# Performance work log

Measured on AMD Instinct MI355X. Metric: run time of the kernel, lower is better.

Reference implementation:

```python
import jax, jax.numpy as jnp
import numpy as np

DIM = 384; H = 64; W = 64; WS = 4; NH = 6; SHIFT = 2
L = WS * WS          # 16 tokens per window
DH = DIM // NH       # 64
SCALE = DH ** -0.5
MLP_H = int(DIM * 4.0)
NW = (H // WS) * (W // WS)


def _ln(x, g, b):
    m = x.mean(-1, keepdims=True)
    v = ((x - m) ** 2).mean(-1, keepdims=True)
    return (x - m) / jnp.sqrt(v + 1e-5) * g + b


def _win(x, B):
    # (B, N, C) -> (B*nW, L, C)
    x = x.reshape(B, H // WS, WS, W // WS, WS, DIM)
    x = x.transpose(0, 1, 3, 2, 4, 5)
    return x.reshape(B * NW, L, DIM)


def _unwin(xw, B):
    # (B*nW, L, C) -> (B, N, C)
    x = xw.reshape(B, H // WS, W // WS, WS, WS, DIM)
    x = x.transpose(0, 1, 3, 2, 4, 5)
    return x.reshape(B, H * W, DIM)


def _build_mask():
    img = np.zeros((H, W))
    slices = [slice(0, -WS), slice(-WS, -SHIFT), slice(-SHIFT, None)]
    cnt = 0
    for hs in slices:
        for ws_ in slices:
            img[hs, ws_] = cnt
            cnt += 1
    mw = img.reshape(H // WS, WS, W // WS, WS).transpose(0, 2, 1, 3).reshape(-1, L)
    am = mw[:, None, :] - mw[:, :, None]          # (nW, L, L)
    am = np.where(am != 0, -100.0, 0.0).astype(np.float32)
    return jnp.asarray(am)

ATTN_MASK = _build_mask()  # (nW, L, L)


def setup_inputs() -> dict:
    key = jax.random.key(0)
    ks = jax.random.split(key, 16)
    n = lambda k, s: jax.random.normal(k, s, jnp.float32) * 0.02
    inp = {
        'x_main': jax.random.normal(ks[0], (16, H * W, DIM), jnp.float32),
        'x_mpmt': jax.random.normal(ks[1], (16, H * W, DIM), jnp.float32),
        'g_q': jnp.ones((DIM,)), 'b_q': jnp.zeros((DIM,)),
        'g_km': jnp.ones((DIM,)), 'b_km': jnp.zeros((DIM,)),
        'g_kp': jnp.ones((DIM,)), 'b_kp': jnp.zeros((DIM,)),
        'Wq': n(ks[2], (DIM, DIM)), 'bq': jnp.zeros((DIM,)),
        'Wk': n(ks[3], (DIM, DIM)), 'bk': jnp.zeros((DIM,)),
        'Wv': n(ks[4], (DIM, DIM)), 'bv': jnp.zeros((DIM,)),
        'Wo': n(ks[5], (DIM, DIM)), 'bo': jnp.zeros((DIM,)),
        'g_mlp': jnp.ones((DIM,)), 'b_mlp': jnp.zeros((DIM,)),
        'W1': n(ks[6], (DIM, MLP_H)), 'b1': jnp.zeros((MLP_H,)),
        'W2': n(ks[7], (MLP_H, DIM)), 'b2': jnp.zeros((DIM,)),
    }
    return inp


def reference(x_main, x_mpmt, g_q, b_q, g_km, b_km, g_kp, b_kp,
              Wq, bq, Wk, bk, Wv, bv, Wo, bo, g_mlp, b_mlp, W1, b1, W2, b2):
    B, N, C = x_main.shape
    q = _ln(x_main, g_q, b_q)
    km = _ln(x_main, g_km, b_km)
    kp = _ln(x_mpmt, g_kp, b_kp)

    roll = lambda t: jnp.roll(t.reshape(B, H, W, C), (-SHIFT, -SHIFT), axis=(1, 2)).reshape(B, N, C)
    q, km, kp = roll(q), roll(km), roll(kp)

    q_w = _win(q, B)                                  # (B*nW, L, C)
    kv_w = jnp.concatenate([_win(km, B), _win(kp, B)], axis=1)  # (B*nW, 2L, C)

    def heads(x, Wm, bm):
        y = x @ Wm + bm
        return y.reshape(y.shape[0], y.shape[1], NH, DH).transpose(0, 2, 1, 3)

    Q = heads(q_w, Wq, bq)    # (B*nW, h, L, dh)
    K = heads(kv_w, Wk, bk)   # (B*nW, h, 2L, dh)
    V = heads(kv_w, Wv, bv)

    scores = jnp.einsum('whqd,whkd->whqk', Q, K) * SCALE   # (B*nW, h, L, 2L)
    mask2 = jnp.concatenate([ATTN_MASK, ATTN_MASK], axis=-1)  # (nW, L, 2L)
    scores = scores.reshape(B, NW, NH, L, 2 * L) + mask2[None, :, None]
    attn = jax.nn.softmax(scores.reshape(B * NW, NH, L, 2 * L), axis=-1)

    out = jnp.einsum('whqk,whkd->whqd', attn, V)           # (B*nW, h, L, dh)
    out = out.transpose(0, 2, 1, 3).reshape(B * NW, L, C)
    y = _unwin(out, B)
    y = jnp.roll(y.reshape(B, H, W, C), (SHIFT, SHIFT), axis=(1, 2)).reshape(B, N, C)

    x = x_main + (y @ Wo + bo)
    xm = _ln(x, g_mlp, b_mlp)
    x = x + (jax.nn.gelu(xm @ W1 + b1, approximate=False) @ W2 + b2)
    return x
```

## Files before the change

kernel.cpp:

```cpp
#include <hip/hip_runtime.h>
#include <cstdint>
#include <cstddef>

#define DEVI __device__ __forceinline__

typedef __attribute__((ext_vector_type(8))) short bf16x8;
typedef __attribute__((ext_vector_type(4))) float f32x4;

DEVI unsigned short f2bf(float f) {
  unsigned u = __builtin_bit_cast(unsigned, f);
  u += 0x7fffu + ((u >> 16) & 1u);
  return (unsigned short)(u >> 16);
}

DEVI f32x4 mfma16(bf16x8 a, bf16x8 b, f32x4 c) {
  return __builtin_amdgcn_mfma_f32_16x16x32_bf16(a, b, c, 0, 0, 0);
}

#define GLD16(g, l) __builtin_amdgcn_global_load_lds( \
    (const __attribute__((address_space(1))) unsigned int*)(g), \
    (__attribute__((address_space(3))) unsigned int*)(l), 16, 0, 0)

__global__ __launch_bounds__(256)
void wtrans_all(const float* __restrict__ Wq, const float* __restrict__ Wk,
                const float* __restrict__ Wv, const float* __restrict__ Wo,
                const float* __restrict__ W1, const float* __restrict__ W2,
                unsigned short* __restrict__ out) {
  int e = blockIdx.x * 256 + threadIdx.x;
  const float* W;
  int K, N, off;
  if (e < 147456) { W = Wq; K = 384; N = 384; off = 0; }
  else if (e < 294912) { W = Wk; K = 384; N = 384; off = 147456; }
  else if (e < 442368) { W = Wv; K = 384; N = 384; off = 294912; }
  else if (e < 589824) { W = Wo; K = 384; N = 384; off = 442368; }
  else if (e < 1179648) { W = W1; K = 384; N = 1536; off = 589824; }
  else { W = W2; K = 1536; N = 384; off = 1179648; }
  int le = e - off;
  int n = le / K, k = le - n * K;
  out[e] = f2bf(W[(size_t)k * N + n]);
}

__global__ __launch_bounds__(256)
void ln_win_k(const float* __restrict__ xm, const float* __restrict__ xp,
              const float* __restrict__ gq, const float* __restrict__ bq,
              const float* __restrict__ gkm, const float* __restrict__ bkm,
              const float* __restrict__ gkp, const float* __restrict__ bkp,
              unsigned short* __restrict__ q_ln,
              unsigned short* __restrict__ kv_ln, int wbase) {
  const int dl = blockIdx.x * 4 + (threadIdx.x >> 6);
  const int l = threadIdx.x & 63;
  const int wl = dl >> 4, t = dl & 15;
  const int w = wbase + wl;
  const int b = w >> 8, wi = w & 255;
  const int hs = (((wi >> 4) << 2) + (t >> 2) + 2) & 63;
  const int ws2 = (((wi & 15) << 2) + (t & 3) + 2) & 63;
  const size_t src = ((size_t)b * 4096 + hs * 64 + ws2) * 384;
  float am[6], ap[6];
  float s1 = 0, s2 = 0, s3 = 0, s4 = 0;
#pragma unroll
  for (int j = 0; j < 6; ++j) {
    am[j] = xm[src + l + j * 64];
    ap[j] = xp[src + l + j * 64];
    s1 += am[j]; s2 += am[j] * am[j];
    s3 += ap[j]; s4 += ap[j] * ap[j];
  }
#pragma unroll
  for (int o = 1; o < 64; o <<= 1) {
    s1 += __shfl_xor(s1, o); s2 += __shfl_xor(s2, o);
    s3 += __shfl_xor(s3, o); s4 += __shfl_xor(s4, o);
  }
  const float mm = s1 * (1.f / 384.f);
  const float vm = s2 * (1.f / 384.f) - mm * mm;
  const float rm = rsqrtf(vm + 1e-5f);
  const float mp = s3 * (1.f / 384.f);
  const float vp = s4 * (1.f / 384.f) - mp * mp;
  const float rp = rsqrtf(vp + 1e-5f);
  unsigned short* qrow = q_ln + (size_t)dl * 384;
  unsigned short* kmrow = kv_ln + ((size_t)wl * 32 + t) * 384;
  unsigned short* kprow = kmrow + 16 * 384;
#pragma unroll
  for (int j = 0; j < 6; ++j) {
    int c = l + j * 64;
    float nm = (am[j] - mm) * rm;
    float np = (ap[j] - mp) * rp;
    qrow[c] = f2bf(nm * gq[c] + bq[c]);
    kmrow[c] = f2bf(nm * gkm[c] + bkm[c]);
    kprow[c] = f2bf(np * gkp[c] + bkp[c]);
  }
}

__global__ __launch_bounds__(256)
void ln_k(const float* __restrict__ x, const float* __restrict__ g,
          const float* __restrict__ b, unsigned short* __restrict__ o) {
  const int row = blockIdx.x * 4 + (threadIdx.x >> 6);
  const int l = threadIdx.x & 63;
  const float* xr = x + (size_t)row * 384;
  float a[6];
  float s1 = 0, s2 = 0;
#pragma unroll
  for (int j = 0; j < 6; ++j) {
    a[j] = xr[l + j * 64];
    s1 += a[j]; s2 += a[j] * a[j];
  }
#pragma unroll
  for (int of = 1; of < 64; of <<= 1) {
    s1 += __shfl_xor(s1, of); s2 += __shfl_xor(s2, of);
  }
  const float m = s1 * (1.f / 384.f);
  const float v = s2 * (1.f / 384.f) - m * m;
  const float r = rsqrtf(v + 1e-5f);
  unsigned short* orow = o + (size_t)row * 384;
#pragma unroll
  for (int j = 0; j < 6; ++j) {
    int c = l + j * 64;
    orow[c] = f2bf((a[j] - m) * r * g[c] + b[c]);
  }
}

enum { EPI_BF16 = 0, EPI_KV = 1, EPI_WO = 2, EPI_GELU = 3, EPI_W2 = 4 };

template <int EPI>
__global__ __launch_bounds__(256, 2)
void gemm_k(const unsigned short* __restrict__ A,
            const unsigned short* __restrict__ Bt,
            const float* __restrict__ bias, const float* __restrict__ bias2,
            void* __restrict__ Cv, void* __restrict__ Cv2,
            const float* __restrict__ extra, int wbase, int M, int N, int K) {
  __shared__ unsigned short As[128 * 32];
  __shared__ unsigned short Bs[128 * 32];
  const int tid = threadIdx.x;
  const int l = tid & 63, wv = tid >> 6;
  const int lr = l & 15, og = l >> 4;

  const unsigned gx = gridDim.x;
  const unsigned nwg = gx * gridDim.y;
  unsigned idx = blockIdx.y * gx + blockIdx.x;
  idx = (idx & 7u) * (nwg >> 3) + (idx >> 3);
  const int m0 = (int)(idx / gx) * 128, n0 = (int)(idx % gx) * 128;

  const int wm = (wv >> 1) * 64, wn = (wv & 1) * 64;

  f32x4 acc[4][4];
#pragma unroll
  for (int i = 0; i < 4; ++i)
#pragma unroll
    for (int j = 0; j < 4; ++j) acc[i][j] = (f32x4){0.f, 0.f, 0.f, 0.f};

  const int r0 = tid >> 2, o0 = (tid & 3) * 8;
  const int r1 = (256 + tid) >> 2, o1 = ((256 + tid) & 3) * 8;
  const unsigned short* a0 = A + (size_t)(m0 + r0) * K + o0;
  const unsigned short* a1 = A + (size_t)(m0 + r1) * K + o1;
  const unsigned short* b0 = Bt + (size_t)(n0 + r0) * K + o0;
  const unsigned short* b1 = Bt + (size_t)(n0 + r1) * K + o1;
  unsigned short* lA0 = &As[(wv * 64) * 8];
  unsigned short* lA1 = &As[(256 + wv * 64) * 8];
  unsigned short* lB0 = &Bs[(wv * 64) * 8];
  unsigned short* lB1 = &Bs[(256 + wv * 64) * 8];

  for (int k0 = 0; k0 < K; k0 += 32) {
    GLD16(a0 + k0, lA0);
    GLD16(a1 + k0, lA1);
    GLD16(b0 + k0, lB0);
    GLD16(b1 + k0, lB1);
    __syncthreads();
    bf16x8 af[4], bfr[4];
#pragma unroll
    for (int i = 0; i < 4; ++i)
      af[i] = *(const bf16x8*)&As[(wm + i * 16 + lr) * 32 + og * 8];
#pragma unroll
    for (int j = 0; j < 4; ++j)
      bfr[j] = *(const bf16x8*)&Bs[(wn + j * 16 + lr) * 32 + og * 8];
#pragma unroll
    for (int i = 0; i < 4; ++i)
#pragma unroll
      for (int j = 0; j < 4; ++j)
        acc[i][j] = mfma16(af[i], bfr[j], acc[i][j]);
    __syncthreads();
  }

#pragma unroll
  for (int j = 0; j < 4; ++j) {
    const int c = n0 + wn + j * 16 + lr;
    const float bv_ =
        (EPI == EPI_KV) ? (c < 384 ? bias[c] : bias2[c - 384]) : bias[c];
#pragma unroll
    for (int i = 0; i < 4; ++i) {
      const int rb = m0 + wm + i * 16 + og * 4;
      if constexpr (EPI == EPI_BF16) {
        unsigned short* C = (unsigned short*)Cv;
#pragma unroll
        for (int r = 0; r < 4; ++r)
          C[(size_t)(rb + r) * N + c] = f2bf(acc[i][j][r] + bv_);
      } else if constexpr (EPI == EPI_KV) {
        if (c < 384) {
          unsigned short* C = (unsigned short*)Cv;
#pragma unroll
          for (int r = 0; r < 4; ++r)
            C[(size_t)(rb + r) * 384 + c] = f2bf(acc[i][j][r] + bv_);
        } else {
          unsigned short* C = (unsigned short*)Cv2;
          int cc = c - 384;
          int wdx = rb >> 5, u = rb & 31;
          size_t ix = (((size_t)wdx * 6 + (cc >> 6)) * 64 + (cc & 63)) * 32 + u;
          ushort4 v4;
          v4.x = f2bf(acc[i][j][0] + bv_);
          v4.y = f2bf(acc[i][j][1] + bv_);
          v4.z = f2bf(acc[i][j][2] + bv_);
          v4.w = f2bf(acc[i][j][3] + bv_);
          *(ushort4*)&C[ix] = v4;
        }
      } else if constexpr (EPI == EPI_WO) {
        float* C = (float*)Cv;
#pragma unroll
        for (int r = 0; r < 4; ++r) {
          int rr = rb + r;
          int wdx = (rr >> 4) + wbase, t = rr & 15;
          int b = wdx >> 8, wi = wdx & 255;
          int hd = (((wi >> 4) << 2) + (t >> 2) + 2) & 63;
          int wd = (((wi & 15) << 2) + (t & 3) + 2) & 63;
          size_t dst = ((size_t)b * 4096 + hd * 64 + wd) * 384 + c;
          C[dst] = extra[dst] + acc[i][j][r] + bv_;
        }
      } else if constexpr (EPI == EPI_GELU) {
        unsigned short* C = (unsigned short*)Cv;
#pragma unroll
        for (int r = 0; r < 4; ++r) {
          float v = acc[i][j][r] + bv_;
          v = 0.5f * v * (1.f + erff(v * 0.70710678118654752f));
          C[(size_t)(rb + r) * N + c] = f2bf(v);
        }
      } else {
        float* C = (float*)Cv;
#pragma unroll
        for (int r = 0; r < 4; ++r) {
          size_t ix = (size_t)(rb + r) * N + c;
          C[ix] = extra[ix] + acc[i][j][r] + bv_;
        }
      }
    }
  }
}

__global__ __launch_bounds__(384)
void attn_k(const unsigned short* __restrict__ Q,
            const unsigned short* __restrict__ K,
            const unsigned short* __restrict__ Vt,
            unsigned short* __restrict__ O, int wbase) {
  __shared__ unsigned short P_lds[6][16][32];
  const int wl = blockIdx.x;
  const int h = threadIdx.x >> 6, l = threadIdx.x & 63;
  const int lr = l & 15, og = l >> 4;
  const int wi = (wbase + wl) & 255;
  const int wh4 = (wi >> 4) << 2, ww4 = (wi & 15) << 2;

  auto rid = [&](int t) -> int {
    int hp = wh4 + (t >> 2), wp = ww4 + (t & 3);
    int rh = hp < 60 ? 0 : (hp < 62 ? 1 : 2);
    int rw = wp < 60 ? 0 : (wp < 62 ? 1 : 2);
    return rh * 3 + rw;
  };
  const int ridq = rid(lr);

  const size_t qbase = ((size_t)wl * 16 + lr) * 384 + h * 64 + og * 8;
  bf16x8 qf0 = *(const bf16x8*)&Q[qbase];
  bf16x8 qf1 = *(const bf16x8*)&Q[qbase + 32];
  const size_t kbase = ((size_t)wl * 32 + lr) * 384 + h * 64 + og * 8;
  bf16x8 kf00 = *(const bf16x8*)&K[kbase];
  bf16x8 kf01 = *(const bf16x8*)&K[kbase + 32];
  bf16x8 kf10 = *(const bf16x8*)&K[kbase + 16 * 384];
  bf16x8 kf11 = *(const bf16x8*)&K[kbase + 16 * 384 + 32];

  f32x4 s0 = (f32x4){0.f, 0.f, 0.f, 0.f}, s1 = (f32x4){0.f, 0.f, 0.f, 0.f};
  s0 = mfma16(kf00, qf0, s0);
  s0 = mfma16(kf01, qf1, s0);
  s1 = mfma16(kf10, qf0, s1);
  s1 = mfma16(kf11, qf1, s1);

  float p[8];
  float mx = -1e30f;
#pragma unroll
  for (int r = 0; r < 4; ++r) {
    float msk = (rid(og * 4 + r) == ridq) ? 0.f : -100.f;
    p[r] = s0[r] * 0.125f + msk;
    p[r + 4] = s1[r] * 0.125f + msk;
    mx = fmaxf(mx, fmaxf(p[r], p[r + 4]));
  }
  mx = fmaxf(mx, __shfl_xor(mx, 16));
  mx = fmaxf(mx, __shfl_xor(mx, 32));
  float sum = 0.f;
#pragma unroll
  for (int r = 0; r < 8; ++r) {
    p[r] = __expf(p[r] - mx);
    sum += p[r];
  }
  sum += __shfl_xor(sum, 16);
  sum += __shfl_xor(sum, 32);
  const float inv = 1.f / sum;

  uint2 pk;
  pk.x = (unsigned)f2bf(p[0] * inv) | ((unsigned)f2bf(p[1] * inv) << 16);
  pk.y = (unsigned)f2bf(p[2] * inv) | ((unsigned)f2bf(p[3] * inv) << 16);
  *(uint2*)&P_lds[h][lr][og * 4] = pk;
  pk.x = (unsigned)f2bf(p[4] * inv) | ((unsigned)f2bf(p[5] * inv) << 16);
  pk.y = (unsigned)f2bf(p[6] * inv) | ((unsigned)f2bf(p[7] * inv) << 16);
  *(uint2*)&P_lds[h][lr][16 + og * 4] = pk;

  bf16x8 pf = *(const bf16x8*)&P_lds[h][lr][og * 8];

  const size_t vbase = (((size_t)wl * 6 + h) * 64 + lr) * 32 + og * 8;
  f32x4 o4[4];
#pragma unroll
  for (int f = 0; f < 4; ++f) {
    bf16x8 vf = *(const bf16x8*)&Vt[vbase + (size_t)f * 16 * 32];
    o4[f] = mfma16(pf, vf, (f32x4){0.f, 0.f, 0.f, 0.f});
  }
#pragma unroll
  for (int f = 0; f < 4; ++f)
#pragma unroll
    for (int r = 0; r < 4; ++r)
      O[((size_t)wl * 16 + og * 4 + r) * 384 + h * 64 + f * 16 + lr] =
          f2bf(o4[f][r]);
}

extern "C" void kernel_launch(void* const* d_in, const int* in_sizes, int n_in,
                              void* d_out, int out_size, void* d_ws,
                              size_t ws_size, hipStream_t stream) {
  const float* x_main = (const float*)d_in[0];
  const float* x_mpmt = (const float*)d_in[1];
  const float* g_q = (const float*)d_in[2];
  const float* b_q = (const float*)d_in[3];
  const float* g_km = (const float*)d_in[4];
  const float* b_km = (const float*)d_in[5];
  const float* g_kp = (const float*)d_in[6];
  const float* b_kp = (const float*)d_in[7];
  const float* Wq = (const float*)d_in[8];
  const float* bq = (const float*)d_in[9];
  const float* Wk = (const float*)d_in[10];
  const float* bk = (const float*)d_in[11];
  const float* Wv = (const float*)d_in[12];
  const float* bv = (const float*)d_in[13];
  const float* Wo = (const float*)d_in[14];
  const float* bo = (const float*)d_in[15];
  const float* g_mlp = (const float*)d_in[16];
  const float* b_mlp = (const float*)d_in[17];
  const float* W1 = (const float*)d_in[18];
  const float* b1 = (const float*)d_in[19];
  const float* W2 = (const float*)d_in[20];
  const float* b2 = (const float*)d_in[21];

  char* ws = (char*)d_ws;
  unsigned short* q_ln = (unsigned short*)(ws + 0);
  unsigned short* Qb = (unsigned short*)(ws + 25165824ull);
  unsigned short* Kb = (unsigned short*)(ws + 50331648ull);
  unsigned short* Vtb = (unsigned short*)(ws + 100663296ull);
  unsigned short* attn_out = q_ln;
  unsigned short* xm = (unsigned short*)(ws + 0);
  unsigned short* Hb = (unsigned short*)(ws + 50331648ull);
  unsigned short* wt = (unsigned short*)(ws + 150994944ull);
  unsigned short* Wqt = wt + 0;
  unsigned short* Wkvt = wt + 147456;
  unsigned short* Wot = wt + 442368;
  unsigned short* W1t = wt + 589824;
  unsigned short* W2t = wt + 1179648;
  float* xout = (float*)d_out;

  wtrans_all<<<6912, 256, 0, stream>>>(Wq, Wk, Wv, Wo, W1, W2, wt);

  for (int c = 0; c < 2; ++c) {
    const int wbase = c * 2048;
    unsigned short* kvl =
        (unsigned short*)((char*)d_out + (size_t)c * 50331648ull);

    ln_win_k<<<8192, 256, 0, stream>>>(x_main, x_mpmt, g_q, b_q, g_km, b_km,
                                       g_kp, b_kp, q_ln, kvl, wbase);

    gemm_k<EPI_BF16><<<dim3(3, 256), 256, 0, stream>>>(
        q_ln, Wqt, bq, nullptr, Qb, nullptr, nullptr, 0, 32768, 384, 384);

    gemm_k<EPI_KV><<<dim3(6, 512), 256, 0, stream>>>(
        kvl, Wkvt, bk, bv, Kb, Vtb, nullptr, 0, 65536, 768, 384);

    attn_k<<<2048, 384, 0, stream>>>(Qb, Kb, Vtb, attn_out, wbase);

    gemm_k<EPI_WO><<<dim3(3, 256), 256, 0, stream>>>(
        attn_out, Wot, bo, nullptr, xout, nullptr, x_main, wbase, 32768, 384,
        384);
  }

  ln_k<<<16384, 256, 0, stream>>>(xout, g_mlp, b_mlp, xm);

  for (int hhalf = 0; hhalf < 2; ++hhalf) {
    const size_t ro = (size_t)hhalf * 32768;
    gemm_k<EPI_GELU><<<dim3(12, 256), 256, 0, stream>>>(
        xm + ro * 384, W1t, b1, nullptr, Hb, nullptr, nullptr, 0, 32768, 1536,
        384);
    gemm_k<EPI_W2><<<dim3(3, 256), 256, 0, stream>>>(
        Hb, W2t, b2, nullptr, xout + ro * 384, nullptr, xout + ro * 384, 0,
        32768, 384, 1536);
  }
}
```

Measured before the change: 998.6 us.

## Double-buffer GEMM LDS tiles, tile weight transpose, reorder epilogue stores

The GEMM main loop now double-buffers the A/B LDS tiles, issuing the next k-slice's global-to-LDS loads before computing on the current one and dropping one barrier per iteration. The weight transpose kernel becomes a 32x32 LDS-tiled transpose so that both reads and writes are coalesced. The epilogues are restructured to hoist bias loads and loop over rows with the column offset innermost. Double-buffering doubles the LDS per block, which may reduce occupancy at launch bounds of 2.

```diff
diff --git a/kernel.cpp b/kernel.cpp
--- a/kernel.cpp
+++ b/kernel.cpp
@@ -26,18 +26,33 @@
                 const float* __restrict__ Wv, const float* __restrict__ Wo,
                 const float* __restrict__ W1, const float* __restrict__ W2,
                 unsigned short* __restrict__ out) {
-  int e = blockIdx.x * 256 + threadIdx.x;
+  __shared__ float tl[32][33];
+  int tu = blockIdx.x;
   const float* W;
-  int K, N, off;
-  if (e < 147456) { W = Wq; K = 384; N = 384; off = 0; }
-  else if (e < 294912) { W = Wk; K = 384; N = 384; off = 147456; }
-  else if (e < 442368) { W = Wv; K = 384; N = 384; off = 294912; }
-  else if (e < 589824) { W = Wo; K = 384; N = 384; off = 442368; }
-  else if (e < 1179648) { W = W1; K = 384; N = 1536; off = 589824; }
-  else { W = W2; K = 1536; N = 384; off = 1179648; }
-  int le = e - off;
-  int n = le / K, k = le - n * K;
-  out[e] = f2bf(W[(size_t)k * N + n]);
+  int K, N, obase;
+  if (tu < 576) {
+    int m = tu / 144;
+    W = (m == 0) ? Wq : (m == 1) ? Wk : (m == 2) ? Wv : Wo;
+    K = 384; N = 384; obase = m * 147456; tu -= m * 144;
+  } else if (tu < 1152) {
+    W = W1; K = 384; N = 1536; obase = 589824; tu -= 576;
+  } else {
+    W = W2; K = 1536; N = 384; obase = 1179648; tu -= 1152;
+  }
+  const int ktiles = K >> 5;
+  const int tn = tu / ktiles, tk = tu - tn * ktiles;
+  const int c = threadIdx.x & 31, rq = threadIdx.x >> 5;
+#pragma unroll
+  for (int ph = 0; ph < 4; ++ph) {
+    int kk = tk * 32 + ph * 8 + rq;
+    tl[ph * 8 + rq][c] = W[(size_t)kk * N + tn * 32 + c];
+  }
+  __syncthreads();
+#pragma unroll
+  for (int ph = 0; ph < 4; ++ph) {
+    int nn = tn * 32 + ph * 8 + rq;
+    out[obase + (size_t)nn * K + tk * 32 + c] = f2bf(tl[c][ph * 8 + rq]);
+  }
 }
 
 __global__ __launch_bounds__(256)
@@ -126,8 +141,8 @@
             const float* __restrict__ bias, const float* __restrict__ bias2,
             void* __restrict__ Cv, void* __restrict__ Cv2,
             const float* __restrict__ extra, int wbase, int M, int N, int K) {
-  __shared__ unsigned short As[128 * 32];
-  __shared__ unsigned short Bs[128 * 32];
+  __shared__ unsigned short As[2][128 * 32];
+  __shared__ unsigned short Bs[2][128 * 32];
   const int tid = threadIdx.x;
   const int l = tid & 63, wv = tid >> 6;
   const int lr = l & 15, og = l >> 4;
@@ -147,29 +162,35 @@
     for (int j = 0; j < 4; ++j) acc[i][j] = (f32x4){0.f, 0.f, 0.f, 0.f};
 
   const int r0 = tid >> 2, o0 = (tid & 3) * 8;
-  const int r1 = (256 + tid) >> 2, o1 = ((256 + tid) & 3) * 8;
   const unsigned short* a0 = A + (size_t)(m0 + r0) * K + o0;
-  const unsigned short* a1 = A + (size_t)(m0 + r1) * K + o1;
+  const unsigned short* a1 = a0 + (size_t)64 * K;
   const unsigned short* b0 = Bt + (size_t)(n0 + r0) * K + o0;
-  const unsigned short* b1 = Bt + (size_t)(n0 + r1) * K + o1;
-  unsigned short* lA0 = &As[(wv * 64) * 8];
-  unsigned short* lA1 = &As[(256 + wv * 64) * 8];
-  unsigned short* lB0 = &Bs[(wv * 64) * 8];
-  unsigned short* lB1 = &Bs[(256 + wv * 64) * 8];
-
-  for (int k0 = 0; k0 < K; k0 += 32) {
-    GLD16(a0 + k0, lA0);
-    GLD16(a1 + k0, lA1);
-    GLD16(b0 + k0, lB0);
-    GLD16(b1 + k0, lB1);
-    __syncthreads();
+  const unsigned short* b1 = b0 + (size_t)64 * K;
+  const int lo = wv * 512;
+
+  const int nk = K >> 5;
+  GLD16(a0, &As[0][lo]);
+  GLD16(a1, &As[0][2048 + lo]);
+  GLD16(b0, &Bs[0][lo]);
+  GLD16(b1, &Bs[0][2048 + lo]);
+  __syncthreads();
+
+  for (int t = 0; t < nk; ++t) {
+    const int cur = t & 1;
+    if (t + 1 < nk) {
+      const int k0 = (t + 1) << 5;
+      GLD16(a0 + k0, &As[cur ^ 1][lo]);
+      GLD16(a1 + k0, &As[cur ^ 1][2048 + lo]);
+      GLD16(b0 + k0, &Bs[cur ^ 1][lo]);
+      GLD16(b1 + k0, &Bs[cur ^ 1][2048 + lo]);
+    }
     bf16x8 af[4], bfr[4];
 #pragma unroll
     for (int i = 0; i < 4; ++i)
-      af[i] = *(const bf16x8*)&As[(wm + i * 16 + lr) * 32 + og * 8];
+      af[i] = *(const bf16x8*)&As[cur][(wm + i * 16 + lr) * 32 + og * 8];
 #pragma unroll
     for (int j = 0; j < 4; ++j)
-      bfr[j] = *(const bf16x8*)&Bs[(wn + j * 16 + lr) * 32 + og * 8];
+      bfr[j] = *(const bf16x8*)&Bs[cur][(wn + j * 16 + lr) * 32 + og * 8];
 #pragma unroll
     for (int i = 0; i < 4; ++i)
 #pragma unroll
@@ -178,63 +199,103 @@
     __syncthreads();
   }
 
+  float bvj[4];
 #pragma unroll
   for (int j = 0; j < 4; ++j) {
-    const int c = n0 + wn + j * 16 + lr;
-    const float bv_ =
-        (EPI == EPI_KV) ? (c < 384 ? bias[c] : bias2[c - 384]) : bias[c];
+    int c = n0 + wn + j * 16 + lr;
+    bvj[j] = (EPI == EPI_KV) ? (c < 384 ? bias[c] : bias2[c - 384]) : bias[c];
+  }
+  const int cb = n0 + wn + lr;
+
+  if constexpr (EPI == EPI_BF16) {
+    unsigned short* C = (unsigned short*)Cv;
 #pragma unroll
     for (int i = 0; i < 4; ++i) {
       const int rb = m0 + wm + i * 16 + og * 4;
-      if constexpr (EPI == EPI_BF16) {
-        unsigned short* C = (unsigned short*)Cv;
-#pragma unroll
-        for (int r = 0; r < 4; ++r)
-          C[(size_t)(rb + r) * N + c] = f2bf(acc[i][j][r] + bv_);
-      } else if constexpr (EPI == EPI_KV) {
-        if (c < 384) {
-          unsigned short* C = (unsigned short*)Cv;
-#pragma unroll
-          for (int r = 0; r < 4; ++r)
-            C[(size_t)(rb + r) * 384 + c] = f2bf(acc[i][j][r] + bv_);
-        } else {
-          unsigned short* C = (unsigned short*)Cv2;
-          int cc = c - 384;
+#pragma unroll
+      for (int r = 0; r < 4; ++r) {
+        unsigned short* row = C + (size_t)(rb + r) * N + cb;
+#pragma unroll
+        for (int j = 0; j < 4; ++j) row[j * 16] = f2bf(acc[i][j][r] + bvj[j]);
+      }
+    }
+  } else if constexpr (EPI == EPI_GELU) {
+    unsigned short* C = (unsigned short*)Cv;
+#pragma unroll
+    for (int i = 0; i < 4; ++i) {
+      const int rb = m0 + wm + i * 16 + og * 4;
+#pragma unroll
+      for (int r = 0; r < 4; ++r) {
+        unsigned short* row = C + (size_t)(rb + r) * N + cb;
+#pragma unroll
+        for (int j = 0; j < 4; ++j) {
+          float v = acc[i][j][r] + bvj[j];
+          v = 0.5f * v * (1.f + erff(v * 0.70710678118654752f));
+          row[j * 16] = f2bf(v);
+        }
+      }
+    }
+  } else if constexpr (EPI == EPI_WO) {
+    float* C = (float*)Cv;
+#pragma unroll
+    for (int i = 0; i < 4; ++i) {
+      const int rb = m0 + wm + i * 16 + og * 4;
+#pragma unroll
+      for (int r = 0; r < 4; ++r) {
+        int rr = rb + r;
+        int wdx = (rr >> 4) + wbase, t = rr & 15;
+        int b = wdx >> 8, wi = wdx & 255;
+        int hd = (((wi >> 4) << 2) + (t >> 2) + 2) & 63;
+        int wd = (((wi & 15) << 2) + (t & 3) + 2) & 63;
+        size_t dst = ((size_t)b * 4096 + hd * 64 + wd) * 384 + cb;
+#pragma unroll
+        for (int j = 0; j < 4; ++j)
+          C[dst + j * 16] = extra[dst + j * 16] + acc[i][j][r] + bvj[j];
+      }
+    }
+  } else if constexpr (EPI == EPI_W2) {
+    float* C = (float*)Cv;
+#pragma unroll
+    for (int i = 0; i < 4; ++i) {
+      const int rb = m0 + wm + i * 16 + og * 4;
+#pragma unroll
+      for (int r = 0; r < 4; ++r) {
+        size_t ix = (size_t)(rb + r) * N + cb;
+#pragma unroll
+        for (int j = 0; j < 4; ++j)
+          C[ix + j * 16] = extra[ix + j * 16] + acc[i][j][r] + bvj[j];
+      }
+    }
+  } else {
+    if (n0 + wn < 384) {
+      unsigned short* C = (unsigned short*)Cv;
+#pragma unroll
+      for (int i = 0; i < 4; ++i) {
+        const int rb = m0 + wm + i * 16 + og * 4;
+#pragma unroll
+        for (int r = 0; r < 4; ++r) {
+          unsigned short* row = C + (size_t)(rb + r) * 384 + cb;
+#pragma unroll
+          for (int j = 0; j < 4; ++j)
+            row[j * 16] = f2bf(acc[i][j][r] + bvj[j]);
+        }
+      }
+    } else {
+      unsigned short* C = (unsigned short*)Cv2;
+#pragma unroll
+      for (int j = 0; j < 4; ++j) {
+        const int cc = n0 + wn + j * 16 + lr - 384;
+#pragma unroll
+        for (int i = 0; i < 4; ++i) {
+          const int rb = m0 + wm + i * 16 + og * 4;
           int wdx = rb >> 5, u = rb & 31;
           size_t ix = (((size_t)wdx * 6 + (cc >> 6)) * 64 + (cc & 63)) * 32 + u;
           ushort4 v4;
-          v4.x = f2bf(acc[i][j][0] + bv_);
-          v4.y = f2bf(acc[i][j][1] + bv_);
-          v4.z = f2bf(acc[i][j][2] + bv_);
-          v4.w = f2bf(acc[i][j][3] + bv_);
+          v4.x = f2bf(acc[i][j][0] + bvj[j]);
+          v4.y = f2bf(acc[i][j][1] + bvj[j]);
+          v4.z = f2bf(acc[i][j][2] + bvj[j]);
+          v4.w = f2bf(acc[i][j][3] + bvj[j]);
           *(ushort4*)&C[ix] = v4;
-        }
-      } else if constexpr (EPI == EPI_WO) {
-        float* C = (float*)Cv;
-#pragma unroll
-        for (int r = 0; r < 4; ++r) {
-          int rr = rb + r;
-          int wdx = (rr >> 4) + wbase, t = rr & 15;
-          int b = wdx >> 8, wi = wdx & 255;
-          int hd = (((wi >> 4) << 2) + (t >> 2) + 2) & 63;
-          int wd = (((wi & 15) << 2) + (t & 3) + 2) & 63;
-          size_t dst = ((size_t)b * 4096 + hd * 64 + wd) * 384 + c;
-          C[dst] = extra[dst] + acc[i][j][r] + bv_;
-        }
-      } else if constexpr (EPI == EPI_GELU) {
-        unsigned short* C = (unsigned short*)Cv;
-#pragma unroll
-        for (int r = 0; r < 4; ++r) {
-          float v = acc[i][j][r] + bv_;
-          v = 0.5f * v * (1.f + erff(v * 0.70710678118654752f));
-          C[(size_t)(rb + r) * N + c] = f2bf(v);
-        }
-      } else {
-        float* C = (float*)Cv;
-#pragma unroll
-        for (int r = 0; r < 4; ++r) {
-          size_t ix = (size_t)(rb + r) * N + c;
-          C[ix] = extra[ix] + acc[i][j][r] + bv_;
         }
       }
     }
@@ -364,7 +425,7 @@
   unsigned short* W2t = wt + 1179648;
   float* xout = (float*)d_out;
 
-  wtrans_all<<<6912, 256, 0, stream>>>(Wq, Wk, Wv, Wo, W1, W2, wt);
+  wtrans_all<<<1728, 256, 0, stream>>>(Wq, Wk, Wv, Wo, W1, W2, wt);
 
   for (int c = 0; c < 2; ++c) {
     const int wbase = c * 2048;
```

After: 823.4 us. 17.5% less time.
